# Optimization experiments

Hardware: AMD Instinct MI355X
Metric: run time of the kernel (lower is better)

Reference implementation:

```python
import jax, jax.numpy as jnp
import numpy as np

DETER, STOCH, ACT, HID, OBS = 1024, 32, 6, 1024, 1024
B, T = 256, 64

def _lin(x, w, b):
    return x @ w.T + b

def setup_inputs() -> dict:
    key = jax.random.key(0)
    ks = iter(jax.random.split(key, 40))
    def p(shape, scale=0.02):
        return (jax.random.normal(next(ks), shape, dtype=jnp.float32) * scale)
    inp = {
        "obs": jax.random.normal(next(ks), (B, T, OBS), dtype=jnp.float32),
        "actions": jax.random.normal(next(ks), (B, T, ACT), dtype=jnp.float32),
        "eps_prior": jax.random.normal(next(ks), (B, T, STOCH), dtype=jnp.float32),
        "eps_post": jax.random.normal(next(ks), (B, T, STOCH), dtype=jnp.float32),
        # input_mlp
        "in_w1": p((HID, STOCH + ACT)), "in_b1": p((HID,)),
        "in_w2": p((HID, HID)), "in_b2": p((HID,)),
        # GRUCell (torch layout: r,z,n chunks)
        "gru_wih": p((3 * DETER, HID)), "gru_whh": p((3 * DETER, DETER)),
        "gru_bih": p((3 * DETER,)), "gru_bhh": p((3 * DETER,)),
        # prior
        "pr_w1": p((HID, DETER)), "pr_b1": p((HID,)),
        "pr_w2": p((HID, HID)), "pr_b2": p((HID,)),
        "pr_mw": p((STOCH, HID)), "pr_mb": p((STOCH,)),
        "pr_sw": p((STOCH, HID)), "pr_sb": p((STOCH,)),
        # posterior
        "po_w1": p((HID, DETER + OBS)), "po_b1": p((HID,)),
        "po_w2": p((HID, HID)), "po_b2": p((HID,)),
        "po_mw": p((STOCH, HID)), "po_mb": p((STOCH,)),
        "po_sw": p((STOCH, HID)), "po_sb": p((STOCH,)),
    }
    return inp

def _rollout(obs, actions, eps_prior, eps_post,
             in_w1, in_b1, in_w2, in_b2,
             gru_wih, gru_whh, gru_bih, gru_bhh,
             pr_w1, pr_b1, pr_w2, pr_b2, pr_mw, pr_mb, pr_sw, pr_sb,
             po_w1, po_b1, po_w2, po_b2, po_mw, po_mb, po_sw, po_sb):
    Bn = obs.shape[0]
    h0 = jnp.zeros((Bn, DETER), obs.dtype)
    z0 = jnp.zeros((Bn, STOCH), obs.dtype)
    a0 = jnp.zeros((Bn, ACT), obs.dtype)

    def step(carry, xs):
        h, z, prev_a = carry
        obs_t, act_t, ep, eq = xs
        x = jnp.concatenate([z, prev_a], axis=-1)
        x = jax.nn.relu(_lin(x, in_w1, in_b1))
        x = jax.nn.relu(_lin(x, in_w2, in_b2))
        # GRUCell
        gi = _lin(x, gru_wih, gru_bih)
        gh = _lin(h, gru_whh, gru_bhh)
        ir, iz, inn = jnp.split(gi, 3, axis=-1)
        hr, hz, hn = jnp.split(gh, 3, axis=-1)
        r = jax.nn.sigmoid(ir + hr)
        u = jax.nn.sigmoid(iz + hz)
        n = jnp.tanh(inn + r * hn)
        h_new = (1.0 - u) * n + u * h
        # prior
        px = jax.nn.relu(_lin(h_new, pr_w1, pr_b1))
        px = jax.nn.relu(_lin(px, pr_w2, pr_b2))
        p_mean = _lin(px, pr_mw, pr_mb)
        p_std = jnp.exp(jnp.clip(_lin(px, pr_sw, pr_sb), -5.0, 2.0))
        # posterior
        qx = jnp.concatenate([h_new, obs_t], axis=-1)
        qx = jax.nn.relu(_lin(qx, po_w1, po_b1))
        qx = jax.nn.relu(_lin(qx, po_w2, po_b2))
        q_mean = _lin(qx, po_mw, po_mb)
        q_std = jnp.exp(jnp.clip(_lin(qx, po_sw, po_sb), -5.0, 2.0))
        z_new = q_mean + q_std * eq
        feat = jnp.concatenate([h_new, z_new], axis=-1)
        return (h_new, z_new, act_t), (feat, p_mean, p_std, q_mean, q_std)

    xs = (jnp.swapaxes(obs, 0, 1), jnp.swapaxes(actions, 0, 1),
          jnp.swapaxes(eps_prior, 0, 1), jnp.swapaxes(eps_post, 0, 1))
    _, (feat, pm, ps, qm, qs) = jax.lax.scan(step, (h0, z0, a0), xs)
    to_bt = lambda a: jnp.swapaxes(a, 0, 1)  # [T,B,...] -> [B,T,...]
    return to_bt(feat), to_bt(pm), to_bt(ps), to_bt(qm), to_bt(qs)

def reference(obs, actions, eps_prior, eps_post,
              in_w1, in_b1, in_w2, in_b2,
              gru_wih, gru_whh, gru_bih, gru_bhh,
              pr_w1, pr_b1, pr_w2, pr_b2, pr_mw, pr_mb, pr_sw, pr_sb,
              po_w1, po_b1, po_w2, po_b2, po_mw, po_mb, po_sw, po_sb):
    return _rollout(obs, actions, eps_prior, eps_post,
                    in_w1, in_b1, in_w2, in_b2,
                    gru_wih, gru_whh, gru_bih, gru_bhh,
                    pr_w1, pr_b1, pr_w2, pr_b2, pr_mw, pr_mb, pr_sw, pr_sb,
                    po_w1, po_b1, po_w2, po_b2, po_mw, po_mb, po_sw, po_sb)
```

## Files before the change

kernel.cpp:

```cpp
#include <hip/hip_runtime.h>
#include <hip/hip_bf16.h>

#define B_   256
#define T_   64
#define OBS_ 1024
#define ACT_ 6
#define STO_ 32
#define HID_ 1024
#define DET_ 1024

using bf16 = __bf16;
typedef __attribute__((ext_vector_type(8))) __bf16 bf16x8;
typedef __attribute__((ext_vector_type(4))) float f32x4;

__device__ __forceinline__ f32x4 MF(bf16x8 a, bf16x8 b, f32x4 c) {
  return __builtin_amdgcn_mfma_f32_16x16x32_bf16(a, b, c, 0, 0, 0);
}

struct CvtArgs {
  const float *in_w2, *gru_wih, *gru_whh, *pr_w1, *pr_w2, *po_w1, *po_w2;
  const float *pr_mw, *pr_sw, *po_mw, *po_sw;
  bf16 *w_in2b, *w_wihb, *w_whhb, *w_pr1b, *w_pr2b, *w_po1hb, *w_po1ob, *w_po2b, *w_headb;
};

__global__ void k_cvtall(CvtArgs a) {
  const int row = blockIdx.x;
  const float* src; bf16* dst; int srcld = 1024, off = 0;
  if      (row < 1024)  { src = a.in_w2   + (size_t)row * 1024;          dst = a.w_in2b  + (size_t)row * 1024; }
  else if (row < 4096)  { int r = row - 1024;  src = a.gru_wih + (size_t)r * 1024; dst = a.w_wihb + (size_t)r * 1024; }
  else if (row < 7168)  { int r = row - 4096;  src = a.gru_whh + (size_t)r * 1024; dst = a.w_whhb + (size_t)r * 1024; }
  else if (row < 8192)  { int r = row - 7168;  src = a.pr_w1   + (size_t)r * 1024; dst = a.w_pr1b + (size_t)r * 1024; }
  else if (row < 9216)  { int r = row - 8192;  src = a.pr_w2   + (size_t)r * 1024; dst = a.w_pr2b + (size_t)r * 1024; }
  else if (row < 10240) { int r = row - 9216;  src = a.po_w1   + (size_t)r * 2048; dst = a.w_po1hb + (size_t)r * 1024; }
  else if (row < 11264) { int r = row - 10240; src = a.po_w1   + (size_t)r * 2048 + 1024; dst = a.w_po1ob + (size_t)r * 1024; }
  else if (row < 12288) { int r = row - 11264; src = a.po_w2   + (size_t)r * 1024; dst = a.w_po2b + (size_t)r * 1024; }
  else {
    int r = row - 12288;
    const float* hs[4] = { a.pr_mw, a.pr_sw, a.po_mw, a.po_sw };
    src = hs[r >> 5] + (size_t)(r & 31) * 1024;
    dst = a.w_headb + (size_t)r * 1024;
  }
  const int c = threadIdx.x * 4;
  float4 f = *(const float4*)(src + c);
  dst[c] = (bf16)f.x; dst[c + 1] = (bf16)f.y; dst[c + 2] = (bf16)f.z; dst[c + 3] = (bf16)f.w;
}

__global__ void k_init(const float* __restrict__ in_b1, bf16* __restrict__ x1b,
                       bf16* __restrict__ hb, float* __restrict__ hf) {
  const int i = blockIdx.x * 256 + threadIdx.x;
  x1b[i] = (bf16)fmaxf(in_b1[i & 1023], 0.f);
  hb[i] = (bf16)0.f;
  hf[i] = 0.f;
}

__global__ __launch_bounds__(256) void k_qbatch(
    const float* __restrict__ obs, const bf16* __restrict__ w,
    const float* __restrict__ bias, float* __restrict__ out) {
  const int tid = threadIdx.x, lane = tid & 63, wv = tid >> 6;
  const int l15 = lane & 15, kg = lane >> 4, kq = kg * 8, rq = kg * 4;
  const int m0 = (blockIdx.x & 255) * 64 + wv * 16;
  const int n0 = (blockIdx.x >> 8) * 64;
  f32x4 c0{0.f,0.f,0.f,0.f}, c1 = c0, c2 = c0, c3 = c0;
  const float* __restrict__ ap = obs + (size_t)(m0 + l15) * 1024 + kq;
  const bf16* __restrict__ wp = w + (size_t)(n0 + l15) * 1024 + kq;
  #pragma unroll 2
  for (int k = 0; k < 1024; k += 32) {
    float4 f0 = *(const float4*)(ap + k);
    float4 f1 = *(const float4*)(ap + k + 4);
    bf16x8 af;
    af[0] = (bf16)f0.x; af[1] = (bf16)f0.y; af[2] = (bf16)f0.z; af[3] = (bf16)f0.w;
    af[4] = (bf16)f1.x; af[5] = (bf16)f1.y; af[6] = (bf16)f1.z; af[7] = (bf16)f1.w;
    c0 = MF(af, *(const bf16x8*)(wp + k            ), c0);
    c1 = MF(af, *(const bf16x8*)(wp + 16 * 1024 + k), c1);
    c2 = MF(af, *(const bf16x8*)(wp + 32 * 1024 + k), c2);
    c3 = MF(af, *(const bf16x8*)(wp + 48 * 1024 + k), c3);
  }
  f32x4 cc[4] = {c0, c1, c2, c3};
  #pragma unroll
  for (int t2 = 0; t2 < 4; ++t2) {
    const int n = n0 + t2 * 16 + l15;
    const float bv = bias[n];
    #pragma unroll
    for (int r = 0; r < 4; ++r)
      out[(size_t)(m0 + rq + r) * 1024 + n] = cc[t2][r] + bv;
  }
}

struct GB {
  const bf16* A;
  const bf16* W;
  const float* bias;
  const float* acc;
  bf16* outB;
  float* outF;
  int N, lda, relu, accStride;
};

__global__ __launch_bounds__(256, 4) void k_mgs(GB g0, GB g1, int s1) {
  GB g; int tile;
  if ((int)blockIdx.x < s1) { g = g0; tile = blockIdx.x; }
  else                      { g = g1; tile = blockIdx.x - s1; }
  __shared__ float sh[3 * 1056];
  const int tid = threadIdx.x, lane = tid & 63, kw = tid >> 6;
  const int l15 = lane & 15, kg = lane >> 4, kq = kg * 8, rq = kg * 4;
  const int m0 = (tile & 15) * 16;
  const int n0 = (tile >> 4) * 64;

  f32x4 c0{0.f,0.f,0.f,0.f}, c1 = c0, c2 = c0, c3 = c0;
  const bf16* __restrict__ ap = g.A + (size_t)(m0 + l15) * g.lda + kw * 256 + kq;
  const bf16* __restrict__ wp = g.W + (size_t)(n0 + l15) * 1024 + kw * 256 + kq;
  #pragma unroll
  for (int k = 0; k < 256; k += 32) {
    bf16x8 af = *(const bf16x8*)(ap + k);
    c0 = MF(af, *(const bf16x8*)(wp + k            ), c0);
    c1 = MF(af, *(const bf16x8*)(wp + 16 * 1024 + k), c1);
    c2 = MF(af, *(const bf16x8*)(wp + 32 * 1024 + k), c2);
    c3 = MF(af, *(const bf16x8*)(wp + 48 * 1024 + k), c3);
  }
  f32x4 cc[4] = {c0, c1, c2, c3};
  if (kw) {
    float* s = sh + (kw - 1) * 1056;
    #pragma unroll
    for (int t2 = 0; t2 < 4; ++t2)
      #pragma unroll
      for (int r = 0; r < 4; ++r)
        s[(rq + r) * 66 + t2 * 16 + l15] = cc[t2][r];
  }
  __syncthreads();
  if (kw == 0) {
    #pragma unroll
    for (int t2 = 0; t2 < 4; ++t2) {
      const int n = n0 + t2 * 16 + l15;
      const float bv = g.bias ? g.bias[n] : 0.f;
      #pragma unroll
      for (int r = 0; r < 4; ++r) {
        const int row = m0 + rq + r;
        float v = cc[t2][r] + bv;
        #pragma unroll
        for (int s = 0; s < 3; ++s)
          v += sh[s * 1056 + (rq + r) * 66 + t2 * 16 + l15];
        if (g.acc) v += g.acc[(size_t)row * g.accStride + n];
        if (g.relu) v = fmaxf(v, 0.f);
        if (g.outB) g.outB[(size_t)row * g.N + n] = (bf16)v;
        if (g.outF) g.outF[(size_t)row * g.N + n] = v;
      }
    }
  }
}

__global__ __launch_bounds__(256, 4) void k_gates2(
    const bf16* __restrict__ x2b, const bf16* __restrict__ wihb,
    const float* __restrict__ bih, const float* __restrict__ gh,
    float* __restrict__ hf, bf16* __restrict__ hb, float* __restrict__ feat, int t) {
  __shared__ float sh[3 * 816];
  const int mt = blockIdx.x & 15, cs = blockIdx.x >> 4;
  const int tid = threadIdx.x, lane = tid & 63, kw = tid >> 6;
  const int l15 = lane & 15, kg = lane >> 4, kq = kg * 8, rq = kg * 4;

  f32x4 ar{0.f,0.f,0.f,0.f}, az = ar, an = ar;
  const bf16* __restrict__ ap = x2b + (size_t)(mt * 16 + l15) * 1024 + kw * 256 + kq;
  const bf16* __restrict__ wr = wihb + (size_t)(cs * 16 + l15) * 1024 + kw * 256 + kq;
  const size_t GOFF = (size_t)1024 * 1024;
  #pragma unroll
  for (int k = 0; k < 256; k += 32) {
    bf16x8 af = *(const bf16x8*)(ap + k);
    ar = MF(af, *(const bf16x8*)(wr + k           ), ar);
    az = MF(af, *(const bf16x8*)(wr + GOFF + k    ), az);
    an = MF(af, *(const bf16x8*)(wr + 2 * GOFF + k), an);
  }
  if (kw) {
    float* s = sh + (kw - 1) * 816;
    #pragma unroll
    for (int r = 0; r < 4; ++r) {
      s[(rq + r) * 17 + l15]             = ar[r];
      s[272 + (rq + r) * 17 + l15]       = az[r];
      s[544 + (rq + r) * 17 + l15]       = an[r];
    }
  }
  __syncthreads();
  if (kw == 0) {
    const int c = cs * 16 + l15;
    const float bir = bih[c], biz = bih[1024 + c], bin_ = bih[2048 + c];
    #pragma unroll
    for (int r = 0; r < 4; ++r) {
      float vr = ar[r], vz = az[r], vn = an[r];
      #pragma unroll
      for (int s = 0; s < 3; ++s) {
        vr += sh[s * 816 + (rq + r) * 17 + l15];
        vz += sh[s * 816 + 272 + (rq + r) * 17 + l15];
        vn += sh[s * 816 + 544 + (rq + r) * 17 + l15];
      }
      const int m = mt * 16 + rq + r;
      const float* ghp = gh + (size_t)m * 3072 + c;
      float rr = vr + bir + ghp[0];
      float zz = vz + biz + ghp[1024];
      const float hn = ghp[2048];
      rr = 1.f / (1.f + __expf(-rr));
      zz = 1.f / (1.f + __expf(-zz));
      const float nn = tanhf(vn + bin_ + rr * hn);
      const float h2 = (1.f - zz) * nn + zz * hf[(size_t)m * 1024 + c];
      hf[(size_t)m * 1024 + c] = h2;
      hb[(size_t)m * 1024 + c] = (bf16)h2;
      feat[((size_t)m * T_ + t) * 1056 + c] = h2;
    }
  }
}

__global__ __launch_bounds__(1024, 1) void k_headfin2(
    const bf16* __restrict__ p2b, const bf16* __restrict__ q2b,
    const bf16* __restrict__ whead,
    const float* __restrict__ pr_mb, const float* __restrict__ pr_sb,
    const float* __restrict__ po_mb, const float* __restrict__ po_sb,
    const float* __restrict__ eps, const float* __restrict__ act,
    const float* __restrict__ in_w1, const float* __restrict__ in_b1,
    float* __restrict__ pm, float* __restrict__ ps,
    float* __restrict__ qm, float* __restrict__ qs,
    float* __restrict__ feat, bf16* __restrict__ x1b, int t) {
  __shared__ float sh[8 * 1056];
  __shared__ float zm[16][32], zs[16][32], zl[16][32], al[16][8];
  const int g = blockIdx.x, m0 = g * 16;
  const int tid = threadIdx.x, lane = tid & 63, w = tid >> 6;
  const int l15 = lane & 15, kg = lane >> 4, kq = kg * 8, rq = kg * 4;

  if (w < 8) {
    const int kw = w & 3, half = w >> 2;
    const bf16* __restrict__ A = half ? q2b : p2b;
    f32x4 c0{0.f,0.f,0.f,0.f}, c1 = c0, c2 = c0, c3 = c0;
    const bf16* __restrict__ ap = A + (size_t)(m0 + l15) * 1024 + kw * 256 + kq;
    const bf16* __restrict__ wp = whead + (size_t)(half * 64 + l15) * 1024 + kw * 256 + kq;
    #pragma unroll
    for (int k = 0; k < 256; k += 32) {
      bf16x8 af = *(const bf16x8*)(ap + k);
      c0 = MF(af, *(const bf16x8*)(wp + k            ), c0);
      c1 = MF(af, *(const bf16x8*)(wp + 16 * 1024 + k), c1);
      c2 = MF(af, *(const bf16x8*)(wp + 32 * 1024 + k), c2);
      c3 = MF(af, *(const bf16x8*)(wp + 48 * 1024 + k), c3);
    }
    f32x4 cc[4] = {c0, c1, c2, c3};
    float* s = sh + w * 1056;
    #pragma unroll
    for (int t2 = 0; t2 < 4; ++t2)
      #pragma unroll
      for (int r = 0; r < 4; ++r)
        s[(rq + r) * 66 + t2 * 16 + l15] = cc[t2][r];
  }
  if (tid >= 928 && tid < 1024) {
    const int idx = tid - 928, r = idx / ACT_, k = idx - r * ACT_;
    al[r][k] = act[((size_t)(m0 + r) * T_ + t) * ACT_ + k];
  }
  __syncthreads();

  #pragma unroll
  for (int rep = 0; rep < 2; ++rep) {
    const int idx = rep * 1024 + tid;
    const int r = idx >> 7, c = idx & 127;
    const int base = (c < 64) ? 0 : 4, cl = c & 63;
    float v = sh[base * 1056 + r * 66 + cl] + sh[(base + 1) * 1056 + r * 66 + cl]
            + sh[(base + 2) * 1056 + r * 66 + cl] + sh[(base + 3) * 1056 + r * 66 + cl];
    const size_t ob = ((size_t)(m0 + r) * T_ + t) * STO_ + (c & 31);
    const int sel = c >> 5;
    if (sel == 0) {
      pm[ob] = v + pr_mb[c];
    } else if (sel == 1) {
      ps[ob] = __expf(fminf(fmaxf(v + pr_sb[c - 32], -5.f), 2.f));
    } else if (sel == 2) {
      const float x = v + po_mb[c - 64];
      qm[ob] = x; zm[r][c - 64] = x;
    } else {
      const float x = __expf(fminf(fmaxf(v + po_sb[c - 96], -5.f), 2.f));
      qs[ob] = x; zs[r][c - 96] = x;
    }
  }
  __syncthreads();
  if (tid < 512) {
    const int r = tid >> 5, j = tid & 31;
    const float z = zm[r][j] + zs[r][j] * eps[((size_t)(m0 + r) * T_ + t) * STO_ + j];
    zl[r][j] = z;
    feat[((size_t)(m0 + r) * T_ + t) * 1056 + 1024 + j] = z;
  }
  __syncthreads();

  const int n = tid;
  float wv_[38];
  #pragma unroll
  for (int j = 0; j < 38; ++j) wv_[j] = in_w1[(size_t)n * 38 + j];
  const float bn = in_b1[n];
  #pragma unroll 2
  for (int r = 0; r < 16; ++r) {
    float a = bn;
    #pragma unroll
    for (int k = 0; k < STO_; ++k) a = fmaf(zl[r][k], wv_[k], a);
    #pragma unroll
    for (int k = 0; k < ACT_; ++k) a = fmaf(al[r][k], wv_[32 + k], a);
    x1b[(size_t)(m0 + r) * 1024 + n] = (bf16)fmaxf(a, 0.f);
  }
}

extern "C" void kernel_launch(void* const* d_in, const int* in_sizes, int n_in,
                              void* d_out, int out_size, void* d_ws, size_t ws_size,
                              hipStream_t stream) {
  (void)in_sizes; (void)n_in; (void)out_size; (void)ws_size;
  const float* obs      = (const float*)d_in[0];
  const float* actions  = (const float*)d_in[1];
  const float* eps_post = (const float*)d_in[3];
  const float* in_w1 = (const float*)d_in[4];
  const float* in_b1 = (const float*)d_in[5];
  const float* in_w2 = (const float*)d_in[6];
  const float* in_b2 = (const float*)d_in[7];
  const float* gru_wih = (const float*)d_in[8];
  const float* gru_whh = (const float*)d_in[9];
  const float* gru_bih = (const float*)d_in[10];
  const float* gru_bhh = (const float*)d_in[11];
  const float* pr_w1 = (const float*)d_in[12];
  const float* pr_b1 = (const float*)d_in[13];
  const float* pr_w2 = (const float*)d_in[14];
  const float* pr_b2 = (const float*)d_in[15];
  const float* pr_mw = (const float*)d_in[16];
  const float* pr_mb = (const float*)d_in[17];
  const float* pr_sw = (const float*)d_in[18];
  const float* pr_sb = (const float*)d_in[19];
  const float* po_w1 = (const float*)d_in[20];
  const float* po_b1 = (const float*)d_in[21];
  const float* po_w2 = (const float*)d_in[22];
  const float* po_b2 = (const float*)d_in[23];
  const float* po_mw = (const float*)d_in[24];
  const float* po_mb = (const float*)d_in[25];
  const float* po_sw = (const float*)d_in[26];
  const float* po_sb = (const float*)d_in[27];

  float* feat = (float*)d_out;
  float* pm = feat + (size_t)B_ * T_ * 1056;
  float* ps = pm + (size_t)B_ * T_ * STO_;
  float* qm = ps + (size_t)B_ * T_ * STO_;
  float* qs = qm + (size_t)B_ * T_ * STO_;

  char* wp_ = (char*)d_ws;
  auto carve = [&](size_t bytes) -> void* {
    void* r = (void*)wp_;
    wp_ += (bytes + 255) & ~(size_t)255;
    return r;
  };
  bf16* w_in2b  = (bf16*)carve((size_t)HID_ * HID_ * 2);
  bf16* w_wihb  = (bf16*)carve((size_t)3 * DET_ * HID_ * 2);
  bf16* w_whhb  = (bf16*)carve((size_t)3 * DET_ * DET_ * 2);
  bf16* w_pr1b  = (bf16*)carve((size_t)HID_ * DET_ * 2);
  bf16* w_pr2b  = (bf16*)carve((size_t)HID_ * HID_ * 2);
  bf16* w_po1hb = (bf16*)carve((size_t)HID_ * DET_ * 2);
  bf16* w_po1ob = (bf16*)carve((size_t)HID_ * OBS_ * 2);
  bf16* w_po2b  = (bf16*)carve((size_t)HID_ * HID_ * 2);
  bf16* w_headb = (bf16*)carve((size_t)128 * HID_ * 2);
  bf16* x1b  = (bf16*)carve((size_t)B_ * HID_ * 2);
  bf16* x2b  = (bf16*)carve((size_t)B_ * HID_ * 2);
  bf16* hb   = (bf16*)carve((size_t)B_ * DET_ * 2);
  bf16* p1b  = (bf16*)carve((size_t)B_ * HID_ * 2);
  bf16* q1b  = (bf16*)carve((size_t)B_ * HID_ * 2);
  bf16* p2b  = (bf16*)carve((size_t)B_ * HID_ * 2);
  bf16* q2b  = (bf16*)carve((size_t)B_ * HID_ * 2);
  float* hf       = (float*)carve((size_t)B_ * DET_ * 4);
  float* gh       = (float*)carve((size_t)B_ * 3 * DET_ * 4);
  float* q1acc    = (float*)carve((size_t)B_ * T_ * HID_ * 4);

  CvtArgs ca = { in_w2, gru_wih, gru_whh, pr_w1, pr_w2, po_w1, po_w2,
                 pr_mw, pr_sw, po_mw, po_sw,
                 w_in2b, w_wihb, w_whhb, w_pr1b, w_pr2b, w_po1hb, w_po1ob, w_po2b, w_headb };
  k_cvtall<<<dim3(12416), dim3(256), 0, stream>>>(ca);
  k_init<<<dim3(1024), dim3(256), 0, stream>>>(in_b1, x1b, hb, hf);
  k_qbatch<<<dim3(4096), dim3(256), 0, stream>>>(obs, w_po1ob, po_b1, q1acc);

  for (int t = 0; t < T_; ++t) {
    GB g_x2 = { x1b, w_in2b, in_b2,   nullptr, x2b, nullptr, 1024, 1024, 1, 0 };
    GB g_gh = { hb,  w_whhb, gru_bhh, nullptr, nullptr, gh, 3072, 1024, 0, 0 };
    k_mgs<<<dim3(1024), dim3(256), 0, stream>>>(g_x2, g_gh, 256);

    k_gates2<<<dim3(1024), dim3(256), 0, stream>>>(x2b, w_wihb, gru_bih, gh, hf, hb, feat, t);

    GB g_pr1 = { hb, w_pr1b,  pr_b1,   nullptr,           p1b, nullptr, 1024, 1024, 1, 0 };
    GB g_q1  = { hb, w_po1hb, nullptr, q1acc + t * 1024,  q1b, nullptr, 1024, 1024, 1, T_ * 1024 };
    k_mgs<<<dim3(512), dim3(256), 0, stream>>>(g_pr1, g_q1, 256);

    GB g_pr2 = { p1b, w_pr2b, pr_b2, nullptr, p2b, nullptr, 1024, 1024, 1, 0 };
    GB g_po2 = { q1b, w_po2b, po_b2, nullptr, q2b, nullptr, 1024, 1024, 1, 0 };
    k_mgs<<<dim3(512), dim3(256), 0, stream>>>(g_pr2, g_po2, 256);

    k_headfin2<<<dim3(16), dim3(1024), 0, stream>>>(
        p2b, q2b, w_headb, pr_mb, pr_sb, po_mb, po_sb,
        eps_post, actions, in_w1, in_b1, pm, ps, qm, qs, feat, x1b, t);
  }
}
```

Before: 6.055 ms.

## Enlarge GEMM block tiles over batch rows to reuse weight fragments across waves

Replaces the 256-thread split-K GEMM kernels with 512-thread templated versions that cover 32 or 64 batch rows per block. Several waves share the same weight columns and split K less finely. This cuts the number of blocks and the redundant weight reads from global/L2, and shrinks the cross-wave shared-memory reduction. The gates kernel is reshaped the same way, with 64 rows per block and a two-way K split. The trade-off is fewer blocks (256) on a many-CU GPU, longer per-wave K loops and fewer resident blocks per CU.

Result: no change. 6.074 ms (+0.3%).

```diff
diff --git a/kernel.cpp b/kernel.cpp
--- a/kernel.cpp
+++ b/kernel.cpp
@@ -25,7 +25,7 @@
 
 __global__ void k_cvtall(CvtArgs a) {
   const int row = blockIdx.x;
-  const float* src; bf16* dst; int srcld = 1024, off = 0;
+  const float* src; bf16* dst;
   if      (row < 1024)  { src = a.in_w2   + (size_t)row * 1024;          dst = a.w_in2b  + (size_t)row * 1024; }
   else if (row < 4096)  { int r = row - 1024;  src = a.gru_wih + (size_t)r * 1024; dst = a.w_wihb + (size_t)r * 1024; }
   else if (row < 7168)  { int r = row - 4096;  src = a.gru_whh + (size_t)r * 1024; dst = a.w_whhb + (size_t)r * 1024; }
@@ -96,21 +96,28 @@
   int N, lda, relu, accStride;
 };
 
-__global__ __launch_bounds__(256, 4) void k_mgs(GB g0, GB g1, int s1) {
+template<int MR>
+__global__ __launch_bounds__(512, 2) void k_mg2(GB g0, GB g1, int s1) {
+  constexpr int NMT  = 256 / MR;
+  constexpr int MSUB = MR / 16;
+  constexpr int RED  = 8 / MSUB;
+  constexpr int KSEG = 1024 / RED;
   GB g; int tile;
   if ((int)blockIdx.x < s1) { g = g0; tile = blockIdx.x; }
   else                      { g = g1; tile = blockIdx.x - s1; }
-  __shared__ float sh[3 * 1056];
-  const int tid = threadIdx.x, lane = tid & 63, kw = tid >> 6;
+  __shared__ float sh[(RED - 1) * MSUB * 1056];
+  const int tid = threadIdx.x, lane = tid & 63, wv = tid >> 6;
+  const int msub = wv & (MSUB - 1), kw = wv / MSUB;
   const int l15 = lane & 15, kg = lane >> 4, kq = kg * 8, rq = kg * 4;
-  const int m0 = (tile & 15) * 16;
-  const int n0 = (tile >> 4) * 64;
+  const int m0 = (tile % NMT) * MR + msub * 16;
+  const int n0 = (tile / NMT) * 64;
+  const int kb = kw * KSEG;
 
   f32x4 c0{0.f,0.f,0.f,0.f}, c1 = c0, c2 = c0, c3 = c0;
-  const bf16* __restrict__ ap = g.A + (size_t)(m0 + l15) * g.lda + kw * 256 + kq;
-  const bf16* __restrict__ wp = g.W + (size_t)(n0 + l15) * 1024 + kw * 256 + kq;
-  #pragma unroll
-  for (int k = 0; k < 256; k += 32) {
+  const bf16* __restrict__ ap = g.A + (size_t)(m0 + l15) * g.lda + kb + kq;
+  const bf16* __restrict__ wp = g.W + (size_t)(n0 + l15) * 1024 + kb + kq;
+  #pragma unroll
+  for (int k = 0; k < KSEG; k += 32) {
     bf16x8 af = *(const bf16x8*)(ap + k);
     c0 = MF(af, *(const bf16x8*)(wp + k            ), c0);
     c1 = MF(af, *(const bf16x8*)(wp + 16 * 1024 + k), c1);
@@ -119,7 +126,7 @@
   }
   f32x4 cc[4] = {c0, c1, c2, c3};
   if (kw) {
-    float* s = sh + (kw - 1) * 1056;
+    float* s = sh + ((kw - 1) * MSUB + msub) * 1056;
     #pragma unroll
     for (int t2 = 0; t2 < 4; ++t2)
       #pragma unroll
@@ -137,8 +144,8 @@
         const int row = m0 + rq + r;
         float v = cc[t2][r] + bv;
         #pragma unroll
-        for (int s = 0; s < 3; ++s)
-          v += sh[s * 1056 + (rq + r) * 66 + t2 * 16 + l15];
+        for (int s = 0; s < RED - 1; ++s)
+          v += sh[(s * MSUB + msub) * 1056 + (rq + r) * 66 + t2 * 16 + l15];
         if (g.acc) v += g.acc[(size_t)row * g.accStride + n];
         if (g.relu) v = fmaxf(v, 0.f);
         if (g.outB) g.outB[(size_t)row * g.N + n] = (bf16)v;
@@ -148,49 +155,48 @@
   }
 }
 
-__global__ __launch_bounds__(256, 4) void k_gates2(
+__global__ __launch_bounds__(512, 2) void k_gates3(
     const bf16* __restrict__ x2b, const bf16* __restrict__ wihb,
     const float* __restrict__ bih, const float* __restrict__ gh,
     float* __restrict__ hf, bf16* __restrict__ hb, float* __restrict__ feat, int t) {
-  __shared__ float sh[3 * 816];
-  const int mt = blockIdx.x & 15, cs = blockIdx.x >> 4;
-  const int tid = threadIdx.x, lane = tid & 63, kw = tid >> 6;
+  __shared__ float sh[4 * 816];
+  const int mt = blockIdx.x & 3, cs = blockIdx.x >> 2;
+  const int tid = threadIdx.x, lane = tid & 63, wv = tid >> 6;
+  const int msub = wv & 3, kw = wv >> 2;
   const int l15 = lane & 15, kg = lane >> 4, kq = kg * 8, rq = kg * 4;
+  const int mrow = mt * 64 + msub * 16;
 
   f32x4 ar{0.f,0.f,0.f,0.f}, az = ar, an = ar;
-  const bf16* __restrict__ ap = x2b + (size_t)(mt * 16 + l15) * 1024 + kw * 256 + kq;
-  const bf16* __restrict__ wr = wihb + (size_t)(cs * 16 + l15) * 1024 + kw * 256 + kq;
+  const bf16* __restrict__ ap = x2b + (size_t)(mrow + l15) * 1024 + kw * 512 + kq;
+  const bf16* __restrict__ wr = wihb + (size_t)(cs * 16 + l15) * 1024 + kw * 512 + kq;
   const size_t GOFF = (size_t)1024 * 1024;
   #pragma unroll
-  for (int k = 0; k < 256; k += 32) {
+  for (int k = 0; k < 512; k += 32) {
     bf16x8 af = *(const bf16x8*)(ap + k);
     ar = MF(af, *(const bf16x8*)(wr + k           ), ar);
     az = MF(af, *(const bf16x8*)(wr + GOFF + k    ), az);
     an = MF(af, *(const bf16x8*)(wr + 2 * GOFF + k), an);
   }
   if (kw) {
-    float* s = sh + (kw - 1) * 816;
+    float* s = sh + msub * 816;
     #pragma unroll
     for (int r = 0; r < 4; ++r) {
-      s[(rq + r) * 17 + l15]             = ar[r];
-      s[272 + (rq + r) * 17 + l15]       = az[r];
-      s[544 + (rq + r) * 17 + l15]       = an[r];
+      s[(rq + r) * 17 + l15]       = ar[r];
+      s[272 + (rq + r) * 17 + l15] = az[r];
+      s[544 + (rq + r) * 17 + l15] = an[r];
     }
   }
   __syncthreads();
   if (kw == 0) {
     const int c = cs * 16 + l15;
     const float bir = bih[c], biz = bih[1024 + c], bin_ = bih[2048 + c];
+    float* s = sh + msub * 816;
     #pragma unroll
     for (int r = 0; r < 4; ++r) {
-      float vr = ar[r], vz = az[r], vn = an[r];
-      #pragma unroll
-      for (int s = 0; s < 3; ++s) {
-        vr += sh[s * 816 + (rq + r) * 17 + l15];
-        vz += sh[s * 816 + 272 + (rq + r) * 17 + l15];
-        vn += sh[s * 816 + 544 + (rq + r) * 17 + l15];
-      }
-      const int m = mt * 16 + rq + r;
+      const float vr = ar[r] + s[(rq + r) * 17 + l15];
+      const float vz = az[r] + s[272 + (rq + r) * 17 + l15];
+      const float vn = an[r] + s[544 + (rq + r) * 17 + l15];
+      const int m = mrow + rq + r;
       const float* ghp = gh + (size_t)m * 3072 + c;
       float rr = vr + bir + ghp[0];
       float zz = vz + biz + ghp[1024];
@@ -356,9 +362,9 @@
   bf16* q1b  = (bf16*)carve((size_t)B_ * HID_ * 2);
   bf16* p2b  = (bf16*)carve((size_t)B_ * HID_ * 2);
   bf16* q2b  = (bf16*)carve((size_t)B_ * HID_ * 2);
-  float* hf       = (float*)carve((size_t)B_ * DET_ * 4);
-  float* gh       = (float*)carve((size_t)B_ * 3 * DET_ * 4);
-  float* q1acc    = (float*)carve((size_t)B_ * T_ * HID_ * 4);
+  float* hf    = (float*)carve((size_t)B_ * DET_ * 4);
+  float* gh    = (float*)carve((size_t)B_ * 3 * DET_ * 4);
+  float* q1acc = (float*)carve((size_t)B_ * T_ * HID_ * 4);
 
   CvtArgs ca = { in_w2, gru_wih, gru_whh, pr_w1, pr_w2, po_w1, po_w2,
                  pr_mw, pr_sw, po_mw, po_sw,
@@ -370,17 +376,17 @@
   for (int t = 0; t < T_; ++t) {
     GB g_x2 = { x1b, w_in2b, in_b2,   nullptr, x2b, nullptr, 1024, 1024, 1, 0 };
     GB g_gh = { hb,  w_whhb, gru_bhh, nullptr, nullptr, gh, 3072, 1024, 0, 0 };
-    k_mgs<<<dim3(1024), dim3(256), 0, stream>>>(g_x2, g_gh, 256);
-
-    k_gates2<<<dim3(1024), dim3(256), 0, stream>>>(x2b, w_wihb, gru_bih, gh, hf, hb, feat, t);
+    k_mg2<64><<<dim3(256), dim3(512), 0, stream>>>(g_x2, g_gh, 64);
+
+    k_gates3<<<dim3(256), dim3(512), 0, stream>>>(x2b, w_wihb, gru_bih, gh, hf, hb, feat, t);
 
     GB g_pr1 = { hb, w_pr1b,  pr_b1,   nullptr,           p1b, nullptr, 1024, 1024, 1, 0 };
     GB g_q1  = { hb, w_po1hb, nullptr, q1acc + t * 1024,  q1b, nullptr, 1024, 1024, 1, T_ * 1024 };
-    k_mgs<<<dim3(512), dim3(256), 0, stream>>>(g_pr1, g_q1, 256);
+    k_mg2<32><<<dim3(256), dim3(512), 0, stream>>>(g_pr1, g_q1, 128);
 
     GB g_pr2 = { p1b, w_pr2b, pr_b2, nullptr, p2b, nullptr, 1024, 1024, 1, 0 };
     GB g_po2 = { q1b, w_po2b, po_b2, nullptr, q2b, nullptr, 1024, 1024, 1, 0 };
-    k_mgs<<<dim3(512), dim3(256), 0, stream>>>(g_pr2, g_po2, 256);
+    k_mg2<32><<<dim3(256), dim3(512), 0, stream>>>(g_pr2, g_po2, 128);
 
     k_headfin2<<<dim3(16), dim3(1024), 0, stream>>>(
         p2b, q2b, w_headb, pr_mb, pr_sb, po_mb, po_sb,
```
